# Kernel tuning notes

Measured on AMD Instinct MI355X. Metric: run time of the kernel, lower is better.

Reference implementation:

```python
import jax, jax.numpy as jnp
import numpy as np

B, S, D = 4, 2048, 1024
H = 16
HD = D // H  # head_dim = 64


def setup_inputs() -> dict:
    key = jax.random.key(0)
    ks = jax.random.split(key, 5)
    scale = 1.0 / np.sqrt(D)
    return {
        "x": jax.random.normal(ks[0], (B, S, D), dtype=jnp.float32),
        "Wq": jax.random.normal(ks[1], (D, D), dtype=jnp.float32) * scale,
        "Wk": jax.random.normal(ks[2], (D, D), dtype=jnp.float32) * scale,
        "Wv": jax.random.normal(ks[3], (D, D), dtype=jnp.float32) * scale,
        "Wo": jax.random.normal(ks[4], (D, D), dtype=jnp.float32) * scale,
        "bo": jnp.zeros((D,), dtype=jnp.float32),
    }


def reference(x, Wq, Wk, Wv, Wo, bo):
    b, s, d = x.shape
    # project and split heads: [b, h, s, hd]
    q = (x @ Wq).reshape(b, s, H, HD).transpose(0, 2, 1, 3)
    k = (x @ Wk).reshape(b, s, H, HD).transpose(0, 2, 1, 3)
    v = (x @ Wv).reshape(b, s, H, HD).transpose(0, 2, 1, 3)
    # scores: [b, h, s, s]
    scores = jnp.einsum("bhqd,bhkd->bhqk", q, k)
    # NOTE: original uses tril(diagonal=1) -> allows one future token (off-by-one)
    mask = jnp.tril(jnp.ones((s, s), dtype=bool), k=1)
    scores = jnp.where(mask, scores, -jnp.inf)
    attn = jax.nn.softmax(scores / np.sqrt(HD), axis=-1)
    # dropout p=0.0 (deterministic baseline): identity
    ctx = jnp.einsum("bhqk,bhkd->bhqd", attn, v)
    ctx = ctx.transpose(0, 2, 1, 3).reshape(b, s, d)
    return ctx @ Wo + bo
```

## Files before the change

kernel.cpp:

```cpp
#include <hip/hip_runtime.h>
#include <hip/hip_bf16.h>

#define Bq 4
#define Sq 2048
#define Dq 1024
#define Hq 16
#define HDq 64
#define Mq (Bq*Sq)

typedef unsigned short u16;
typedef __attribute__((ext_vector_type(8))) __bf16 b16x8;
typedef __attribute__((ext_vector_type(4))) float f32x4;
typedef __attribute__((ext_vector_type(4))) unsigned int u32x4;

__device__ inline float bf2f(u16 h){ union{unsigned u; float f;} v; v.u = ((unsigned)h)<<16; return v.f; }
__device__ inline u16 f2bf(float f){ union{float f; unsigned u;} v; v.f=f; unsigned r = v.u + 0x7FFFu + ((v.u>>16)&1u); return (u16)(r>>16); }
__device__ inline u16 truncbf(float f){ union{float f; unsigned u;} v; v.f=f; return (u16)(v.u>>16); }
__device__ inline float ld_elem(const void* p, size_t i, int isf32){
  return isf32 ? ((const float*)p)[i] : bf2f(((const u16*)p)[i]);
}
__device__ inline void ld16(const u16* g, u16* l){
  __builtin_amdgcn_global_load_lds((const __attribute__((address_space(1))) void*)g,
                                   (__attribute__((address_space(3))) void*)l, 16, 0, 0);
}

#if __has_builtin(__builtin_amdgcn_exp2f)
#define EXP2(x) __builtin_amdgcn_exp2f(x)
#else
#define EXP2(x) __expf((x)*0.69314718056f)
#endif
#define SCALE_LOG2E 0.18033688011112042f

__device__ inline int detect_wave(const unsigned* __restrict__ x, int t){
  unsigned w = x[t & 255];
  unsigned long long m1 = __ballot(((w>>7)&0xFFu)>=0x90u);
  unsigned long long m2 = __ballot(((w>>23)&0xFFu)>=0x90u);
  return (__popcll(m1)+__popcll(m2)) > 8 ? 1 : 0;
}

__global__ __launch_bounds__(256) void prep(
    const void* __restrict__ x,
    const void* __restrict__ W0, const void* __restrict__ W1,
    const void* __restrict__ W2, const void* __restrict__ W3,
    u16* __restrict__ xc,
    u16* __restrict__ T0, u16* __restrict__ T1,
    u16* __restrict__ T2, u16* __restrict__ T3){
  __shared__ u16 tile[64][65];
  const int t = threadIdx.x;
  const int f = detect_wave((const unsigned*)x, t);
  const int bid = blockIdx.x;
  if (bid < 4096){
    int i = (bid*256 + t)*8;
    if(f){
      const float* xf=(const float*)x;
      #pragma unroll
      for(int j=0;j<8;j++) xc[i+j] = f2bf(xf[i+j]);
    } else {
      *(u32x4*)&xc[i] = *(const u32x4*)((const u16*)x + i);
    }
  } else {
    int idx = bid - 4096;
    int z = idx >> 8, rem = idx & 255;
    int k0 = (rem & 15)*64, n0 = (rem >> 4)*64;
    const void* src = (z==0)?W0:(z==1)?W1:(z==2)?W2:W3;
    u16*       dst = (z==0)?T0:(z==1)?T1:(z==2)?T2:T3;
    #pragma unroll
    for(int r=0;r<16;r++){
      int row = r*4 + (t>>6), col = t&63;
      tile[row][col] = f2bf(ld_elem(src, (size_t)(k0+row)*Dq + n0 + col, f));
    }
    __syncthreads();
    #pragma unroll
    for(int r=0;r<16;r++){
      int row = r*4 + (t>>6), col = t&63;
      dst[(size_t)(n0+row)*Dq + k0 + col] = tile[col][row];
    }
  }
}

__global__ __launch_bounds__(512, 4) void gemm_qkv(
    const u16* __restrict__ A, const u16* __restrict__ Bt,
    u16* __restrict__ O0, u16* __restrict__ O1, u16* __restrict__ O2){
  constexpr int NT = Dq/32;
  __shared__ u16 Asl[2][256*32];
  __shared__ u16 Bsl[2][128*32];
  const int t = threadIdx.x;
  const int lane = t & 63, wave = t >> 6;
  const int quad = lane >> 4, l16 = lane & 15;
  const int wr = wave >> 1, wc = wave & 1;
  int L = blockIdx.x + blockIdx.y*gridDim.x;
  int k8 = L & 7, ii = L >> 3;
  int nsb = ii >> 5, rem = ii & 31;
  int mg = rem >> 3, ng = rem & 7;
  const int m0 = (k8*4 + mg)*256, n0 = (nsb*8 + ng)*128;

  f32x4 acc[4][4] = {};

  auto stage = [&](int T, int s){
    #pragma unroll
    for(int r=0;r<2;r++){
      int idx = t + (r<<9);
      int row = idx>>2, g = idx&3;
      int gl = g ^ ((row>>1)&3);
      ld16(&A[(size_t)(m0+row)*Dq + (T<<5) + gl*8], &Asl[s][idx*8]);
    }
    { int idx = t;
      int row = idx>>2, g = idx&3;
      int gl = g ^ ((row>>1)&3);
      ld16(&Bt[(size_t)(n0+row)*Dq + (T<<5) + gl*8], &Bsl[s][idx*8]); }
  };
  auto ldA = [&](int s, int i)->b16x8{
    int row = wr*64 + i*16 + l16;
    return *(const b16x8*)&Asl[s][row*32 + ((quad ^ ((row>>1)&3))<<3)];
  };
  auto ldB = [&](int s, int j)->b16x8{
    int row = wc*64 + j*16 + l16;
    return *(const b16x8*)&Bsl[s][row*32 + ((quad ^ ((row>>1)&3))<<3)];
  };
  #define MFMA_BF16 __builtin_amdgcn_mfma_f32_16x16x32_bf16

  stage(0, 0);

  for(int tt=0; tt<NT; ++tt){
    const int s = tt&1;
    if(tt+1<NT){
      stage(tt+1, s^1);
      asm volatile("s_waitcnt vmcnt(3)" ::: "memory");
    } else {
      asm volatile("s_waitcnt vmcnt(0)" ::: "memory");
    }
    __builtin_amdgcn_s_barrier();
    __builtin_amdgcn_sched_barrier(0);
    b16x8 af[4], bf[4];
    #pragma unroll
    for(int i=0;i<4;i++) af[i]=ldA(s,i);
    #pragma unroll
    for(int j=0;j<4;j++) bf[j]=ldB(s,j);
    asm volatile("s_waitcnt lgkmcnt(0)" ::: "memory");
    __builtin_amdgcn_sched_barrier(0);
    __builtin_amdgcn_s_setprio(1);
    #pragma unroll
    for(int i=0;i<4;i++)
      #pragma unroll
      for(int j=0;j<4;j++)
        acc[i][j]=MFMA_BF16(af[i],bf[j],acc[i][j],0,0,0);
    __builtin_amdgcn_s_setprio(0);
    __builtin_amdgcn_s_barrier();
    __builtin_amdgcn_sched_barrier(0);
  }

  #pragma unroll
  for(int i=0;i<4;i++){
    #pragma unroll
    for(int j=0;j<4;j++){
      int n = n0 + wc*64 + j*16 + l16;
      #pragma unroll
      for(int r=0;r<4;r++){
        int m = m0 + wr*64 + i*16 + quad*4 + r;
        float c = acc[i][j][r];
        int z = n >> 10, nn2 = n & 1023;
        int b = m >> 11, s2x = m & 2047;
        int h = nn2 >> 6, hd = nn2 & 63;
        if (z==0)      O0[(((size_t)(b*Hq + h))*Sq + s2x)*HDq + hd] = f2bf(c*SCALE_LOG2E);
        else if (z==1) O1[(((size_t)(b*Hq + h))*Sq + s2x)*HDq + hd] = f2bf(c);
        else           O2[(((size_t)(b*Hq + h))*HDq + hd)*Sq + s2x] = f2bf(c);
      }
    }
  }
  #undef MFMA_BF16
}

__global__ __launch_bounds__(256, 3) void gemm_op(
    const u16* __restrict__ A, const u16* __restrict__ Bt,
    void* __restrict__ Og, const void* __restrict__ bias,
    const unsigned* __restrict__ xdet){
  constexpr int NT = Dq/32;
  __shared__ u16 Asl[3][128*32];
  __shared__ u16 Bsl[3][128*32];
  const int f = detect_wave(xdet, threadIdx.x);
  const int t = threadIdx.x;
  const int lane = t & 63, wave = t >> 6;
  const int quad = lane >> 4, l16 = lane & 15;
  const int wr = wave >> 1, wc = wave & 1;
  int L = blockIdx.x + blockIdx.y*gridDim.x;
  int k8 = L & 7, ii = L >> 3;
  int mg = ii >> 3, ng = ii & 7;
  const int m0 = (k8*8 + mg)*128, n0 = ng*128;

  f32x4 acc[4][4] = {};

  auto stageA = [&](int T, int s){
    #pragma unroll
    for(int r=0;r<2;r++){
      int idx = t + (r<<8);
      int row = idx>>2, g = idx&3;
      int gl = g ^ ((row>>1)&3);
      ld16(&A[(size_t)(m0+row)*Dq + (T<<5) + gl*8], &Asl[s][idx*8]);
    }
  };
  auto stageB = [&](int T, int s){
    #pragma unroll
    for(int r=0;r<2;r++){
      int idx = t + (r<<8);
      int row = idx>>2, g = idx&3;
      int gl = g ^ ((row>>1)&3);
      ld16(&Bt[(size_t)(n0+row)*Dq + (T<<5) + gl*8], &Bsl[s][idx*8]);
    }
  };
  auto ldA = [&](int s, int i)->b16x8{
    int row = wr*64 + i*16 + l16;
    return *(const b16x8*)&Asl[s][row*32 + ((quad ^ ((row>>1)&3))<<3)];
  };
  auto ldB = [&](int s, int j)->b16x8{
    int row = wc*64 + j*16 + l16;
    return *(const b16x8*)&Bsl[s][row*32 + ((quad ^ ((row>>1)&3))<<3)];
  };
  #define MFMA_BF16 __builtin_amdgcn_mfma_f32_16x16x32_bf16

  stageA(0,0); stageB(0,0); stageA(1,1); stageB(1,1);
  asm volatile("s_waitcnt vmcnt(4)" ::: "memory");
  __builtin_amdgcn_s_barrier();
  __builtin_amdgcn_sched_barrier(0);

  int s0=0, s1=1, s2=2;
  for(int tt=0; tt<NT; ++tt){
    if(tt+2<NT){ stageA(tt+2, s2); stageB(tt+2, s2); }
    b16x8 af[4], bf[4];
    #pragma unroll
    for(int i=0;i<4;i++) af[i]=ldA(s0,i);
    #pragma unroll
    for(int j=0;j<4;j++) bf[j]=ldB(s0,j);
    __builtin_amdgcn_s_barrier();
    asm volatile("s_waitcnt lgkmcnt(0)" ::: "memory");
    __builtin_amdgcn_sched_barrier(0);
    __builtin_amdgcn_s_setprio(1);
    #pragma unroll
    for(int i=0;i<4;i++)
      #pragma unroll
      for(int j=0;j<4;j++)
        acc[i][j]=MFMA_BF16(af[i],bf[j],acc[i][j],0,0,0);
    __builtin_amdgcn_s_setprio(0);
    if(tt<NT-2) asm volatile("s_waitcnt vmcnt(4)" ::: "memory");
    else        asm volatile("s_waitcnt vmcnt(0)" ::: "memory");
    __builtin_amdgcn_s_barrier();
    __builtin_amdgcn_sched_barrier(0);
    int x2=s0; s0=s1; s1=s2; s2=x2;
  }

  #pragma unroll
  for(int i=0;i<4;i++){
    #pragma unroll
    for(int j=0;j<4;j++){
      int n = n0 + wc*64 + j*16 + l16;
      #pragma unroll
      for(int r=0;r<4;r++){
        int m = m0 + wr*64 + i*16 + quad*4 + r;
        float c2 = acc[i][j][r] + ld_elem(bias, n, f);
        if (f) ((float*)Og)[(size_t)m*Dq + n] = c2;
        else   ((u16*)Og)[(size_t)m*Dq + n]   = f2bf(c2);
      }
    }
  }
  #undef MFMA_BF16
}

__global__ __launch_bounds__(256) void flash_attn(
    const u16* __restrict__ Q, const u16* __restrict__ K,
    const u16* __restrict__ VT, u16* __restrict__ C){
  __shared__ u16 Kt[128*64];
  __shared__ u16 Vt[64*128];
  __shared__ u16 Pl[4][16][72];
  const int t = threadIdx.x;
  const int lane = t&63, wave = t>>6, quad = lane>>4, l16 = lane&15;
  int L  = blockIdx.x + blockIdx.y*gridDim.x;
  int k8 = L & 7, ii = L >> 3;
  const int bh = k8*8 + (ii>>4);
  const int p  = ii & 15;
  const int b = bh >> 4, h = bh & 15;
  const int qt[2] = { p, 31 - p };
  int nk[2];
  #pragma unroll
  for(int tt=0;tt<2;tt++){ int v = qt[tt]+2; nk[tt] = (v<32)?v:32; }
  const int nrounds = (nk[1]+1)>>1;
  const u16* Qh = Q  + (size_t)bh*Sq*HDq;
  const u16* Kh = K  + (size_t)bh*Sq*HDq;
  const u16* Vh = VT + (size_t)bh*HDq*Sq;

  b16x8 aq[2][2];
  #pragma unroll
  for(int tt=0;tt<2;tt++){
    const u16* qp = Qh + (size_t)(qt[tt]*64 + wave*16 + l16)*HDq + quad*8;
    aq[tt][0] = *(const b16x8*)qp;
    aq[tt][1] = *(const b16x8*)(qp + 32);
  }
  b16x8 vone;
  #pragma unroll
  for(int i=0;i<8;i++) vone[i] = (__bf16)1.0f;

  const f32x4 fzero = {0.f,0.f,0.f,0.f};
  f32x4 Oa[2][4]; f32x4 lacc[2];
  #pragma unroll
  for(int tt=0;tt<2;tt++){ lacc[tt]=fzero; for(int j=0;j<4;j++) Oa[tt][j]=fzero; }

  for(int kt2=0; kt2<nrounds; kt2++){
    __syncthreads();
    #pragma unroll
    for(int r=0;r<4;r++){
      int idx = t + (r<<8);
      int row = idx>>3, g = idx&7;
      int csw = (g ^ (row&7))<<3;
      ld16(Kh + (size_t)(kt2*128+row)*HDq + csw, Kt + idx*8);
    }
    #pragma unroll
    for(int r=0;r<4;r++){
      int idx = t + (r<<8);
      int row = idx>>4, g = idx&15;
      int csw = (g ^ (row&15))<<3;
      ld16(Vh + (size_t)row*Sq + (size_t)kt2*128 + csw, Vt + idx*8);
    }
    __syncthreads();

    #pragma unroll
    for(int half=0; half<2; half++){
      const int kt = kt2*2 + half;
      #pragma unroll
      for(int tt=0;tt<2;tt++){
        if (kt >= nk[tt]) continue;
        const int qq0 = qt[tt]*64;
        f32x4 sc[4];
        #pragma unroll
        for(int jn=0;jn<4;jn++){
          int krow = half*64 + jn*16 + l16;
          const u16* kp = &Kt[krow*64];
          f32x4 s = fzero;
          b16x8 bk0 = *(const b16x8*)&kp[((quad     ^ (krow&7))<<3)];
          b16x8 bk1 = *(const b16x8*)&kp[(((quad+4) ^ (krow&7))<<3)];
          s = __builtin_amdgcn_mfma_f32_16x16x32_bf16(aq[tt][0], bk0, s, 0,0,0);
          s = __builtin_amdgcn_mfma_f32_16x16x32_bf16(aq[tt][1], bk1, s, 0,0,0);
          sc[jn] = s;
        }
        if (kt < qt[tt]) {
          #pragma unroll
          for(int jn=0;jn<4;jn++)
            #pragma unroll
            for(int r=0;r<4;r++)
              Pl[wave][quad*4+r][jn*16+l16] = truncbf(EXP2(sc[jn][r]));
        } else {
          const int qbase = qq0 + wave*16 + quad*4;
          #pragma unroll
          for(int jn=0;jn<4;jn++){
            int kg = kt*64 + jn*16 + l16;
            #pragma unroll
            for(int r=0;r<4;r++){
              float sv = sc[jn][r];
              if (kg > qbase + r + 1) sv = -__builtin_inff();
              Pl[wave][quad*4+r][jn*16+l16] = truncbf(EXP2(sv));
            }
          }
        }
        #pragma unroll
        for(int ks=0;ks<2;ks++){
          b16x8 ap = *(const b16x8*)&Pl[wave][l16][ks*32 + quad*8];
          int glog = half*8 + ks*4 + quad;
          #pragma unroll
          for(int jd=0;jd<4;jd++){
            int hd = jd*16 + l16;
            b16x8 bv = *(const b16x8*)&Vt[hd*128 + ((glog ^ (hd&15))<<3)];
            Oa[tt][jd] = __builtin_amdgcn_mfma_f32_16x16x32_bf16(ap, bv, Oa[tt][jd], 0,0,0);
          }
          lacc[tt] = __builtin_amdgcn_mfma_f32_16x16x32_bf16(ap, vone, lacc[tt], 0,0,0);
        }
      }
    }
  }
  #pragma unroll
  for(int tt=0;tt<2;tt++){
    const int qq0 = qt[tt]*64;
    #pragma unroll
    for(int r=0;r<4;r++){
      int s = qq0 + wave*16 + quad*4 + r;
      float inv = 1.0f / lacc[tt][r];
      #pragma unroll
      for(int jd=0;jd<4;jd++)
        C[((size_t)(b*Sq + s))*Dq + h*HDq + jd*16 + l16] = f2bf(Oa[tt][jd][r]*inv);
    }
  }
}

extern "C" void kernel_launch(void* const* d_in, const int* in_sizes, int n_in,
                              void* d_out, int out_size, void* d_ws, size_t ws_size,
                              hipStream_t stream){
  const void* x  = d_in[0];
  const void* Wq = d_in[1];
  const void* Wk = d_in[2];
  const void* Wv = d_in[3];
  const void* Wo = d_in[4];
  const void* bo = d_in[5];

  char* ws = (char*)d_ws;
  size_t off = 0;
  auto wsalloc = [&](size_t bytes)->void*{
    void* p = ws + off; off += (bytes + 255) & ~(size_t)255; return p;
  };
  u16* WqT = (u16*)wsalloc((size_t)Dq*Dq*2);
  u16* WkT = (u16*)wsalloc((size_t)Dq*Dq*2);
  u16* WvT = (u16*)wsalloc((size_t)Dq*Dq*2);
  u16* WoT = (u16*)wsalloc((size_t)Dq*Dq*2);
  u16* xc  = (u16*)wsalloc((size_t)Mq*Dq*2);
  u16* Qb  = (u16*)wsalloc((size_t)Mq*Dq*2);
  u16* Kb  = (u16*)wsalloc((size_t)Mq*Dq*2);
  u16* VTb = (u16*)wsalloc((size_t)Mq*Dq*2);
  u16* Cb  = (u16*)wsalloc((size_t)Mq*Dq*2);

  prep<<<dim3(5120), 256, 0, stream>>>(x, Wq,Wk,Wv,Wo, xc, WqT,WkT,WvT,WoT);
  gemm_qkv<<<dim3(12, 64), 512, 0, stream>>>(xc, WqT, Qb,Kb,VTb);
  flash_attn<<<dim3(16, Bq*Hq), 256, 0, stream>>>(Qb, Kb, VTb, Cb);
  gemm_op<<<dim3(8, 64), 256, 0, stream>>>(Cb, WoT, d_out, bo, (const unsigned*)x);
}
```

Before: 195.0 us.

## Use single-wave 128x128 QKV GEMM tiles and four query tiles per attention block

```diff
diff --git a/kernel.cpp b/kernel.cpp
--- a/kernel.cpp
+++ b/kernel.cpp
@@ -78,85 +78,83 @@
   }
 }
 
-__global__ __launch_bounds__(512, 4) void gemm_qkv(
+__global__ __launch_bounds__(64) void gemm_1w(
     const u16* __restrict__ A, const u16* __restrict__ Bt,
     u16* __restrict__ O0, u16* __restrict__ O1, u16* __restrict__ O2){
   constexpr int NT = Dq/32;
-  __shared__ u16 Asl[2][256*32];
+  __shared__ u16 Asl[2][128*32];
   __shared__ u16 Bsl[2][128*32];
-  const int t = threadIdx.x;
-  const int lane = t & 63, wave = t >> 6;
+  const int lane = threadIdx.x;
   const int quad = lane >> 4, l16 = lane & 15;
-  const int wr = wave >> 1, wc = wave & 1;
   int L = blockIdx.x + blockIdx.y*gridDim.x;
   int k8 = L & 7, ii = L >> 3;
-  int nsb = ii >> 5, rem = ii & 31;
+  int nsb = ii >> 6, rem = ii & 63;
   int mg = rem >> 3, ng = rem & 7;
-  const int m0 = (k8*4 + mg)*256, n0 = (nsb*8 + ng)*128;
-
-  f32x4 acc[4][4] = {};
-
-  auto stage = [&](int T, int s){
-    #pragma unroll
-    for(int r=0;r<2;r++){
-      int idx = t + (r<<9);
+  const int m0 = (k8*8 + mg)*128, n0 = (nsb*8 + ng)*128;
+
+  f32x4 acc[8][8] = {};
+
+  auto stageA = [&](int T, int s){
+    #pragma unroll
+    for(int r=0;r<8;r++){
+      int idx = lane + (r<<6);
       int row = idx>>2, g = idx&3;
       int gl = g ^ ((row>>1)&3);
       ld16(&A[(size_t)(m0+row)*Dq + (T<<5) + gl*8], &Asl[s][idx*8]);
     }
-    { int idx = t;
+  };
+  auto stageB = [&](int T, int s){
+    #pragma unroll
+    for(int r=0;r<8;r++){
+      int idx = lane + (r<<6);
       int row = idx>>2, g = idx&3;
       int gl = g ^ ((row>>1)&3);
-      ld16(&Bt[(size_t)(n0+row)*Dq + (T<<5) + gl*8], &Bsl[s][idx*8]); }
+      ld16(&Bt[(size_t)(n0+row)*Dq + (T<<5) + gl*8], &Bsl[s][idx*8]);
+    }
   };
   auto ldA = [&](int s, int i)->b16x8{
-    int row = wr*64 + i*16 + l16;
+    int row = i*16 + l16;
     return *(const b16x8*)&Asl[s][row*32 + ((quad ^ ((row>>1)&3))<<3)];
   };
   auto ldB = [&](int s, int j)->b16x8{
-    int row = wc*64 + j*16 + l16;
+    int row = j*16 + l16;
     return *(const b16x8*)&Bsl[s][row*32 + ((quad ^ ((row>>1)&3))<<3)];
   };
   #define MFMA_BF16 __builtin_amdgcn_mfma_f32_16x16x32_bf16
 
-  stage(0, 0);
+  stageA(0,0); stageB(0,0);
 
   for(int tt=0; tt<NT; ++tt){
     const int s = tt&1;
     if(tt+1<NT){
-      stage(tt+1, s^1);
-      asm volatile("s_waitcnt vmcnt(3)" ::: "memory");
+      stageA(tt+1, s^1); stageB(tt+1, s^1);
+      asm volatile("s_waitcnt vmcnt(16)" ::: "memory");
     } else {
       asm volatile("s_waitcnt vmcnt(0)" ::: "memory");
     }
-    __builtin_amdgcn_s_barrier();
     __builtin_amdgcn_sched_barrier(0);
-    b16x8 af[4], bf[4];
-    #pragma unroll
-    for(int i=0;i<4;i++) af[i]=ldA(s,i);
-    #pragma unroll
-    for(int j=0;j<4;j++) bf[j]=ldB(s,j);
+    b16x8 af[8], bf[8];
+    #pragma unroll
+    for(int i=0;i<8;i++) af[i]=ldA(s,i);
+    #pragma unroll
+    for(int j=0;j<8;j++) bf[j]=ldB(s,j);
     asm volatile("s_waitcnt lgkmcnt(0)" ::: "memory");
     __builtin_amdgcn_sched_barrier(0);
-    __builtin_amdgcn_s_setprio(1);
-    #pragma unroll
-    for(int i=0;i<4;i++)
-      #pragma unroll
-      for(int j=0;j<4;j++)
+    #pragma unroll
+    for(int i=0;i<8;i++)
+      #pragma unroll
+      for(int j=0;j<8;j++)
         acc[i][j]=MFMA_BF16(af[i],bf[j],acc[i][j],0,0,0);
-    __builtin_amdgcn_s_setprio(0);
-    __builtin_amdgcn_s_barrier();
-    __builtin_amdgcn_sched_barrier(0);
-  }
-
-  #pragma unroll
-  for(int i=0;i<4;i++){
-    #pragma unroll
-    for(int j=0;j<4;j++){
-      int n = n0 + wc*64 + j*16 + l16;
+  }
+
+  #pragma unroll
+  for(int i=0;i<8;i++){
+    #pragma unroll
+    for(int j=0;j<8;j++){
+      int n = n0 + j*16 + l16;
       #pragma unroll
       for(int r=0;r<4;r++){
-        int m = m0 + wr*64 + i*16 + quad*4 + r;
+        int m = m0 + i*16 + quad*4 + r;
         float c = acc[i][j][r];
         int z = n >> 10, nn2 = n & 1023;
         int b = m >> 11, s2x = m & 2047;
@@ -274,21 +272,21 @@
   const int lane = t&63, wave = t>>6, quad = lane>>4, l16 = lane&15;
   int L  = blockIdx.x + blockIdx.y*gridDim.x;
   int k8 = L & 7, ii = L >> 3;
-  const int bh = k8*8 + (ii>>4);
-  const int p  = ii & 15;
+  const int bh = k8*8 + (ii>>3);
+  const int p  = ii & 7;
   const int b = bh >> 4, h = bh & 15;
-  const int qt[2] = { p, 31 - p };
-  int nk[2];
-  #pragma unroll
-  for(int tt=0;tt<2;tt++){ int v = qt[tt]+2; nk[tt] = (v<32)?v:32; }
-  const int nrounds = (nk[1]+1)>>1;
+  const int qt[4] = { p, 15-p, 16+p, 31-p };
+  int nk[4];
+  #pragma unroll
+  for(int tt=0;tt<4;tt++){ int v = qt[tt]+2; nk[tt] = (v<32)?v:32; }
+  const int nrounds = (nk[3]+1)>>1;
   const u16* Qh = Q  + (size_t)bh*Sq*HDq;
   const u16* Kh = K  + (size_t)bh*Sq*HDq;
   const u16* Vh = VT + (size_t)bh*HDq*Sq;
 
-  b16x8 aq[2][2];
-  #pragma unroll
-  for(int tt=0;tt<2;tt++){
+  b16x8 aq[4][2];
+  #pragma unroll
+  for(int tt=0;tt<4;tt++){
     const u16* qp = Qh + (size_t)(qt[tt]*64 + wave*16 + l16)*HDq + quad*8;
     aq[tt][0] = *(const b16x8*)qp;
     aq[tt][1] = *(const b16x8*)(qp + 32);
@@ -298,9 +296,9 @@
   for(int i=0;i<8;i++) vone[i] = (__bf16)1.0f;
 
   const f32x4 fzero = {0.f,0.f,0.f,0.f};
-  f32x4 Oa[2][4]; f32x4 lacc[2];
-  #pragma unroll
-  for(int tt=0;tt<2;tt++){ lacc[tt]=fzero; for(int j=0;j<4;j++) Oa[tt][j]=fzero; }
+  f32x4 Oa[4][4]; f32x4 lacc[4];
+  #pragma unroll
+  for(int tt=0;tt<4;tt++){ lacc[tt]=fzero; for(int j=0;j<4;j++) Oa[tt][j]=fzero; }
 
   for(int kt2=0; kt2<nrounds; kt2++){
     __syncthreads();
@@ -324,7 +322,7 @@
     for(int half=0; half<2; half++){
       const int kt = kt2*2 + half;
       #pragma unroll
-      for(int tt=0;tt<2;tt++){
+      for(int tt=0;tt<4;tt++){
         if (kt >= nk[tt]) continue;
         const int qq0 = qt[tt]*64;
         f32x4 sc[4];
@@ -374,7 +372,7 @@
     }
   }
   #pragma unroll
-  for(int tt=0;tt<2;tt++){
+  for(int tt=0;tt<4;tt++){
     const int qq0 = qt[tt]*64;
     #pragma unroll
     for(int r=0;r<4;r++){
@@ -413,7 +411,7 @@
   u16* Cb  = (u16*)wsalloc((size_t)Mq*Dq*2);
 
   prep<<<dim3(5120), 256, 0, stream>>>(x, Wq,Wk,Wv,Wo, xc, WqT,WkT,WvT,WoT);
-  gemm_qkv<<<dim3(12, 64), 512, 0, stream>>>(xc, WqT, Qb,Kb,VTb);
-  flash_attn<<<dim3(16, Bq*Hq), 256, 0, stream>>>(Qb, Kb, VTb, Cb);
+  gemm_1w<<<dim3(24, 64), 64, 0, stream>>>(xc, WqT, Qb,Kb,VTb);
+  flash_attn<<<dim3(8, Bq*Hq), 256, 0, stream>>>(Qb, Kb, VTb, Cb);
   gemm_op<<<dim3(8, 64), 256, 0, stream>>>(Cb, WoT, d_out, bo, (const unsigned*)x);
 }
```

Result: slower. 238.1 us (+22.1%).
